# Kernel tuning notes

Hardware: AMD Instinct MI355X
Metric: run time of the kernel (lower is better)

Reference implementation:

```python
import math
import jax, jax.numpy as jnp
import numpy as np

NUM_HEADS = 12
KEEP_RATE = 0.7


def setup_inputs() -> dict:
    key = jax.random.key(0)
    k1, k2, k3 = jax.random.split(key, 3)
    B, N, C = 16, 577, 768
    x = jax.random.normal(k1, (B, N, C), dtype=jnp.float32)
    qkv_w = jax.random.normal(k2, (3 * C, C), dtype=jnp.float32) * 0.02
    proj_w = jax.random.normal(k3, (C, C), dtype=jnp.float32) * 0.02
    proj_b = jnp.zeros((C,), dtype=jnp.float32)
    return {"x": x, "qkv_w": qkv_w, "proj_w": proj_w, "proj_b": proj_b}


def reference(x, qkv_w, proj_w, proj_b):
    B, N, C = x.shape
    H = NUM_HEADS
    hd = C // H
    scale = hd ** -0.5
    # qkv projection (no bias): [B, N, 3C] -> [3, B, H, N, hd]
    qkv = (x @ qkv_w.T).reshape(B, N, 3, H, hd).transpose(2, 0, 3, 1, 4)
    q, k, v = qkv[0], qkv[1], qkv[2]
    attn = jax.nn.softmax(jnp.einsum('bhnd,bhmd->bhnm', q, k) * scale, axis=-1)
    out = jnp.einsum('bhnm,bhmd->bhnd', attn, v)          # [B,H,N,hd]
    out = out.transpose(0, 2, 1, 3).reshape(B, N, C)
    out = out @ proj_w.T + proj_b
    # CLS-token attention pruning (keep_rate < 1.0, return_idx=True path)
    left_tokens = math.ceil(KEEP_RATE * (N - 1))
    cls_attn = attn[:, :, 0, 1:].mean(axis=1)             # [B, N-1], mean over heads
    _, idx = jax.lax.top_k(cls_attn, left_tokens)         # sorted descending
    index = jnp.broadcast_to(idx[:, :, None], (B, left_tokens, C))
    return out, idx, index, cls_attn
```

## Files before the change

kernel.cpp:

```cpp
#include <hip/hip_runtime.h>
#include <math.h>

#define BB 16
#define NN 577
#define CC 768
#define HH 12
#define HD 64
#define MM (BB*NN)
#define MPAD 9344
#define LEFT 404
#define NPAD 608
#define NQT 10

typedef __attribute__((ext_vector_type(8))) short short8v;
typedef __attribute__((ext_vector_type(4))) float f32x4;

__device__ __forceinline__ unsigned short f2bf(float f) {
    union { float f; unsigned int u; } v; v.f = f;
    unsigned int r = v.u + 0x7fffu + ((v.u >> 16) & 1u);
    return (unsigned short)(r >> 16);
}

__global__ __launch_bounds__(256) void k_gemm_fp32(const float* __restrict__ X,
                                                   const float* __restrict__ W,
                                                   float* __restrict__ kb,
                                                   unsigned short* __restrict__ kbh)
{
    __shared__ float Xs[16][128];
    __shared__ float Ws[16][128];
    const int t  = threadIdx.x;
    const int tx = t & 15, ty = t >> 4;
    const int m0 = blockIdx.x * 128;
    const int n0 = 768 + blockIdx.y * 128;
    const int sm = t & 127;
    const int sk = (t >> 7) * 8;

    float acc[8][8];
    #pragma unroll
    for (int i = 0; i < 8; ++i)
        #pragma unroll
        for (int j = 0; j < 8; ++j) acc[i][j] = 0.f;

    const int gm = m0 + sm;
    const float* px = X + (size_t)gm * CC + sk;
    const float* pw = W + (size_t)(n0 + sm) * CC + sk;

    float4 a0 = make_float4(0.f,0.f,0.f,0.f), a1 = a0, b0, b1;
    if (gm < MM) { a0 = *(const float4*)px; a1 = *(const float4*)(px + 4); }
    b0 = *(const float4*)pw; b1 = *(const float4*)(pw + 4);

    for (int kk = 0; kk < CC; kk += 16) {
        Xs[sk+0][sm] = a0.x; Xs[sk+1][sm] = a0.y; Xs[sk+2][sm] = a0.z; Xs[sk+3][sm] = a0.w;
        Xs[sk+4][sm] = a1.x; Xs[sk+5][sm] = a1.y; Xs[sk+6][sm] = a1.z; Xs[sk+7][sm] = a1.w;
        Ws[sk+0][sm] = b0.x; Ws[sk+1][sm] = b0.y; Ws[sk+2][sm] = b0.z; Ws[sk+3][sm] = b0.w;
        Ws[sk+4][sm] = b1.x; Ws[sk+5][sm] = b1.y; Ws[sk+6][sm] = b1.z; Ws[sk+7][sm] = b1.w;
        __syncthreads();
        if (kk + 16 < CC) {
            a0 = make_float4(0.f,0.f,0.f,0.f); a1 = a0;
            if (gm < MM) { a0 = *(const float4*)(px + kk + 16); a1 = *(const float4*)(px + kk + 20); }
            b0 = *(const float4*)(pw + kk + 16); b1 = *(const float4*)(pw + kk + 20);
        }
        #pragma unroll
        for (int k = 0; k < 16; ++k) {
            float a[8], bv[8];
            *(float4*)&a[0]  = *(const float4*)&Xs[k][ty*4];
            *(float4*)&a[4]  = *(const float4*)&Xs[k][64 + ty*4];
            *(float4*)&bv[0] = *(const float4*)&Ws[k][tx*4];
            *(float4*)&bv[4] = *(const float4*)&Ws[k][64 + tx*4];
            #pragma unroll
            for (int i = 0; i < 8; ++i)
                #pragma unroll
                for (int j = 0; j < 8; ++j)
                    acc[i][j] = fmaf(a[i], bv[j], acc[i][j]);
        }
        __syncthreads();
    }
    #pragma unroll
    for (int i = 0; i < 8; ++i) {
        const int mrow = m0 + ((i < 4) ? (ty*4 + i) : (64 + ty*4 + i - 4));
        if (mrow >= MM) continue;
        const int b_ = mrow / NN;
        const int n_ = mrow - b_ * NN;
        #pragma unroll
        for (int j = 0; j < 8; ++j) {
            const int col = (n0 - 768) + ((j < 4) ? (tx*4 + j) : (64 + tx*4 + j - 4));
            const int h = col >> 6, d = col & 63;
            const float a = acc[i][j];
            kb [(((size_t)b_ * HH + h) * NN   + n_) * HD + d] = a;
            kbh[(((size_t)b_ * HH + h) * NPAD + n_) * HD + d] = f2bf(a);
        }
    }
}

__global__ __launch_bounds__(256) void qcls_kernel(const float* __restrict__ X,
                                                   const float* __restrict__ W,
                                                   float* __restrict__ qcls)
{
    const int b = blockIdx.x;
    const int col = blockIdx.y * 256 + threadIdx.x;
    const float* xr = X + (size_t)b * NN * CC;
    const float* wr = W + (size_t)col * CC;
    float acc = 0.f;
    for (int k = 0; k < CC; ++k) acc = fmaf(xr[k], wr[k], acc);
    qcls[(size_t)b * CC + col] = acc;
}

#define N4X 1772544
#define N4W 442368
#define N4P 147456
__global__ __launch_bounds__(256) void convert3(const float* __restrict__ x,
                                                const float* __restrict__ wq,
                                                const float* __restrict__ wp,
                                                unsigned short* __restrict__ xb,
                                                unsigned short* __restrict__ wqb,
                                                unsigned short* __restrict__ wpb)
{
    int g = blockIdx.x * 256 + threadIdx.x;
    const float* src; unsigned short* dst;
    if (g < N4X)            { src = x;  dst = xb;  }
    else if (g < N4X + N4W) { g -= N4X; src = wq; dst = wqb; }
    else                    { g -= (N4X + N4W); src = wp; dst = wpb; }
    const float4 v = ((const float4*)src)[g];
    ushort4 o;
    o.x = f2bf(v.x); o.y = f2bf(v.y); o.z = f2bf(v.z); o.w = f2bf(v.w);
    ((ushort4*)dst)[g] = o;
}

__global__ __launch_bounds__(256) void qv_mfma(const unsigned short* __restrict__ xbh,
                                               const unsigned short* __restrict__ wqkv,
                                               unsigned short* __restrict__ qbh,
                                               unsigned short* __restrict__ Vt)
{
    __shared__ unsigned short As[128*32];
    __shared__ unsigned short Bs[128*32];
    const int t = threadIdx.x;
    const int w = t >> 6, l = t & 63;
    const int l15 = l & 15, lk = l >> 4;
    const int wm = w >> 1, wn = w & 1;
    const int m0 = blockIdx.x * 128;
    const int isV = blockIdx.y >= 6;
    const int nlocal0 = (isV ? (blockIdx.y - 6) : blockIdx.y) * 128;
    const int wrow0 = (isV ? 1536 : 0) + nlocal0;
    const int r0 = t >> 2, segp = t & 3;

    f32x4 acc[4][4];
    #pragma unroll
    for (int i = 0; i < 4; ++i)
        #pragma unroll
        for (int j = 0; j < 4; ++j) acc[i][j] = (f32x4){0.f,0.f,0.f,0.f};

    const unsigned short* ga = xbh  + (size_t)(m0 + r0) * CC + segp * 8;
    const unsigned short* gb = wqkv + (size_t)(wrow0 + r0) * CC + segp * 8;

    for (int kk = 0; kk < CC; kk += 32) {
        const short8v a0 = *(const short8v*)(ga + kk);
        const short8v a1 = *(const short8v*)(ga + kk + (size_t)64 * CC);
        const short8v b0 = *(const short8v*)(gb + kk);
        const short8v b1 = *(const short8v*)(gb + kk + (size_t)64 * CC);
        __syncthreads();
        *(short8v*)&As[(r0)      * 32 + segp*8] = a0;
        *(short8v*)&As[(64 + r0) * 32 + segp*8] = a1;
        *(short8v*)&Bs[(r0)      * 32 + segp*8] = b0;
        *(short8v*)&Bs[(64 + r0) * 32 + segp*8] = b1;
        __syncthreads();
        short8v fa[4], fb[4];
        #pragma unroll
        for (int i = 0; i < 4; ++i) fa[i] = *(const short8v*)&As[(wm*64 + i*16 + l15)*32 + lk*8];
        #pragma unroll
        for (int j = 0; j < 4; ++j) fb[j] = *(const short8v*)&Bs[(wn*64 + j*16 + l15)*32 + lk*8];
        #pragma unroll
        for (int i = 0; i < 4; ++i)
            #pragma unroll
            for (int j = 0; j < 4; ++j)
                acc[i][j] = __builtin_amdgcn_mfma_f32_16x16x32_bf16(fa[i], fb[j], acc[i][j], 0, 0, 0);
    }

    const int nb = nlocal0 + wn*64 + l15;
    #pragma unroll
    for (int i = 0; i < 4; ++i) {
        #pragma unroll
        for (int r = 0; r < 4; ++r) {
            const int m = m0 + wm*64 + i*16 + 4*lk + r;
            if (m >= MM) continue;
            const int b_ = m / NN, tok = m - b_ * NN;
            #pragma unroll
            for (int j = 0; j < 4; ++j) {
                const int nl = nb + j*16;
                const int h = nl >> 6, d = nl & 63;
                const unsigned short v = f2bf(acc[i][j][r]);
                if (isV) Vt [(((size_t)b_*HH + h)*HD + d)*NPAD + tok] = v;
                else     qbh[(((size_t)b_*HH + h)*NPAD + tok)*HD + d] = v;
            }
        }
    }
}

__global__ __launch_bounds__(256) void proj_mfma(const unsigned short* __restrict__ aobh,
                                                 const unsigned short* __restrict__ wpb,
                                                 const float* __restrict__ bias,
                                                 float* __restrict__ outp)
{
    __shared__ unsigned short As[128*32];
    __shared__ unsigned short Bs[128*32];
    const int t = threadIdx.x;
    const int w = t >> 6, l = t & 63;
    const int l15 = l & 15, lk = l >> 4;
    const int wm = w >> 1, wn = w & 1;
    const int m0 = blockIdx.x * 128;
    const int n0 = blockIdx.y * 128;
    const int r0 = t >> 2, segp = t & 3;

    f32x4 acc[4][4];
    #pragma unroll
    for (int i = 0; i < 4; ++i)
        #pragma unroll
        for (int j = 0; j < 4; ++j) acc[i][j] = (f32x4){0.f,0.f,0.f,0.f};

    const unsigned short* ga = aobh + (size_t)(m0 + r0) * CC + segp * 8;
    const unsigned short* gb = wpb  + (size_t)(n0 + r0) * CC + segp * 8;

    for (int kk = 0; kk < CC; kk += 32) {
        const short8v a0 = *(const short8v*)(ga + kk);
        const short8v a1 = *(const short8v*)(ga + kk + (size_t)64 * CC);
        const short8v b0 = *(const short8v*)(gb + kk);
        const short8v b1 = *(const short8v*)(gb + kk + (size_t)64 * CC);
        __syncthreads();
        *(short8v*)&As[(r0)      * 32 + segp*8] = a0;
        *(short8v*)&As[(64 + r0) * 32 + segp*8] = a1;
        *(short8v*)&Bs[(r0)      * 32 + segp*8] = b0;
        *(short8v*)&Bs[(64 + r0) * 32 + segp*8] = b1;
        __syncthreads();
        short8v fa[4], fb[4];
        #pragma unroll
        for (int i = 0; i < 4; ++i) fa[i] = *(const short8v*)&As[(wm*64 + i*16 + l15)*32 + lk*8];
        #pragma unroll
        for (int j = 0; j < 4; ++j) fb[j] = *(const short8v*)&Bs[(wn*64 + j*16 + l15)*32 + lk*8];
        #pragma unroll
        for (int i = 0; i < 4; ++i)
            #pragma unroll
            for (int j = 0; j < 4; ++j)
                acc[i][j] = __builtin_amdgcn_mfma_f32_16x16x32_bf16(fa[i], fb[j], acc[i][j], 0, 0, 0);
    }

    const int nb = n0 + wn*64 + l15;
    #pragma unroll
    for (int i = 0; i < 4; ++i) {
        #pragma unroll
        for (int r = 0; r < 4; ++r) {
            const int m = m0 + wm*64 + i*16 + 4*lk + r;
            if (m >= MM) continue;
            #pragma unroll
            for (int j = 0; j < 4; ++j) {
                const int n = nb + j*16;
                outp[(size_t)m * CC + n] = acc[i][j][r] + bias[n];
            }
        }
    }
}

__global__ __launch_bounds__(256) void attn_mfma(const unsigned short* __restrict__ qbh,
                                                 const unsigned short* __restrict__ kbh,
                                                 const unsigned short* __restrict__ Vt,
                                                 unsigned short* __restrict__ aobh)
{
    __shared__ __align__(16) unsigned short plds[4][16][32];
    const int bid = blockIdx.x;
    const int bh  = bid / NQT;
    const int qt  = bid - bh * NQT;
    const int b   = bh / HH, h = bh - b * HH;
    const int t   = threadIdx.x;
    const int w   = t >> 6, l = t & 63;
    const int l15 = l & 15, lg = l >> 4;

    short8v aq0, aq1;
    {
        int qrow = qt*64 + w*16 + l15; if (qrow > 576) qrow = 576;
        const unsigned short* qp = qbh + ((size_t)bh * NPAD + qrow) * HD + lg*8;
        aq0 = *(const short8v*)(qp);
        aq1 = *(const short8v*)(qp + 32);
    }

    f32x4 O0 = {0.f,0.f,0.f,0.f}, O1 = O0, O2 = O0, O3 = O0;
    float mr[4] = {-1e30f,-1e30f,-1e30f,-1e30f};
    float lr[4] = {0.f,0.f,0.f,0.f};

    const unsigned short* kwb = kbh + (size_t)bh * NPAD * HD + (size_t)l15 * HD + lg*8;
    const unsigned short* vwb = Vt  + (size_t)bh * HD * NPAD + (size_t)l15 * NPAD + lg*8;

    for (int c = 0; c < 19; ++c) {
        const int n0 = c * 32;
        const unsigned short* kp = kwb + (size_t)n0 * HD;
        short8v bk00 = *(const short8v*)(kp);
        short8v bk01 = *(const short8v*)(kp + 32);
        short8v bk10 = *(const short8v*)(kp + 16*HD);
        short8v bk11 = *(const short8v*)(kp + 16*HD + 32);
        f32x4 s0 = {0.f,0.f,0.f,0.f}, s1 = {0.f,0.f,0.f,0.f};
        s0 = __builtin_amdgcn_mfma_f32_16x16x32_bf16(aq0, bk00, s0, 0, 0, 0);
        s0 = __builtin_amdgcn_mfma_f32_16x16x32_bf16(aq1, bk01, s0, 0, 0, 0);
        s1 = __builtin_amdgcn_mfma_f32_16x16x32_bf16(aq0, bk10, s1, 0, 0, 0);
        s1 = __builtin_amdgcn_mfma_f32_16x16x32_bf16(aq1, bk11, s1, 0, 0, 0);

        const int nc0 = n0 + l15;
        float p0[4], p1[4], al[4];
        #pragma unroll
        for (int r = 0; r < 4; ++r) {
            float a0 = (nc0      <= 576) ? s0[r] * 0.125f : -1e30f;
            float a1 = (nc0 + 16 <= 576) ? s1[r] * 0.125f : -1e30f;
            float tm = fmaxf(a0, a1);
            tm = fmaxf(tm, __shfl_xor(tm, 1, 64));
            tm = fmaxf(tm, __shfl_xor(tm, 2, 64));
            tm = fmaxf(tm, __shfl_xor(tm, 4, 64));
            tm = fmaxf(tm, __shfl_xor(tm, 8, 64));
            const float mn = fmaxf(mr[r], tm);
            al[r] = __expf(mr[r] - mn);
            mr[r] = mn;
            p0[r] = __expf(a0 - mn);
            p1[r] = __expf(a1 - mn);
            float ps = p0[r] + p1[r];
            ps += __shfl_xor(ps, 1, 64);
            ps += __shfl_xor(ps, 2, 64);
            ps += __shfl_xor(ps, 4, 64);
            ps += __shfl_xor(ps, 8, 64);
            lr[r] = lr[r] * al[r] + ps;
        }
        #pragma unroll
        for (int r = 0; r < 4; ++r) {
            O0[r] *= al[r]; O1[r] *= al[r]; O2[r] *= al[r]; O3[r] *= al[r];
        }
        #pragma unroll
        for (int r = 0; r < 4; ++r) {
            plds[w][lg*4 + r][l15]      = f2bf(p0[r]);
            plds[w][lg*4 + r][16 + l15] = f2bf(p1[r]);
        }
        asm volatile("s_waitcnt lgkmcnt(0)" ::: "memory");
        short8v pa = *(const short8v*)&plds[w][l15][lg*8];
        const unsigned short* vp = vwb + n0;
        short8v v0 = *(const short8v*)(vp);
        short8v v1 = *(const short8v*)(vp + 16*NPAD);
        short8v v2 = *(const short8v*)(vp + 32*NPAD);
        short8v v3 = *(const short8v*)(vp + 48*NPAD);
        O0 = __builtin_amdgcn_mfma_f32_16x16x32_bf16(pa, v0, O0, 0, 0, 0);
        O1 = __builtin_amdgcn_mfma_f32_16x16x32_bf16(pa, v1, O1, 0, 0, 0);
        O2 = __builtin_amdgcn_mfma_f32_16x16x32_bf16(pa, v2, O2, 0, 0, 0);
        O3 = __builtin_amdgcn_mfma_f32_16x16x32_bf16(pa, v3, O3, 0, 0, 0);
    }

    #pragma unroll
    for (int r = 0; r < 4; ++r) {
        const float inv = 1.f / lr[r];
        const int row = qt*64 + w*16 + lg*4 + r;
        if (row <= 576) {
            unsigned short* op = aobh + ((size_t)b * NN + row) * CC + h*HD + l15;
            op[0]  = f2bf(O0[r] * inv);
            op[16] = f2bf(O1[r] * inv);
            op[32] = f2bf(O2[r] * inv);
            op[48] = f2bf(O3[r] * inv);
        }
    }
}

__global__ __launch_bounds__(256) void cls_logits(const float* __restrict__ qcls,
                                                  const float* __restrict__ kb,
                                                  float* __restrict__ P)
{
    const int bh = blockIdx.x;
    const int t = threadIdx.x;
    __shared__ float q[64];
    if (t < 64) q[t] = qcls[(size_t)bh * 64 + t];
    __syncthreads();
    const int n = blockIdx.y * 193 + t;
    if (t < 193 && n < NN) {
        const float* kr = kb + ((size_t)bh * NN + n) * HD;
        float acc = 0.f;
        #pragma unroll
        for (int d = 0; d < 64; ++d) acc = fmaf(q[d], kr[d], acc);
        P[(size_t)bh * NN + n] = acc * 0.125f;
    }
}

__global__ __launch_bounds__(256) void cls_softmax(float* __restrict__ P)
{
    const int bh = blockIdx.x;
    const int t = threadIdx.x;
    float* L = P + (size_t)bh * NN;
    __shared__ float red[256];
    float lmax = -1e30f;
    for (int n = t; n < NN; n += 256) lmax = fmaxf(lmax, L[n]);
    red[t] = lmax; __syncthreads();
    for (int s = 128; s > 0; s >>= 1) { if (t < s) red[t] = fmaxf(red[t], red[t+s]); __syncthreads(); }
    const float m = red[0]; __syncthreads();
    float z = 0.f;
    for (int n = t; n < NN; n += 256) z += expf(L[n] - m);
    red[t] = z; __syncthreads();
    for (int s = 128; s > 0; s >>= 1) { if (t < s) red[t] += red[t+s]; __syncthreads(); }
    const float Z = red[0];
    for (int n = t; n < NN; n += 256) L[n] = expf(L[n] - m) / Z;
}

__global__ __launch_bounds__(256) void cls_meantopk(const float* __restrict__ P,
                                                    float* __restrict__ out_cls,
                                                    float* __restrict__ out_idx,
                                                    int* __restrict__ idxi)
{
    const int b = blockIdx.x;
    const int t = threadIdx.x;
    __shared__ float sv[576];
    for (int j = t; j < 576; j += 256) {
        float s = 0.f;
        #pragma unroll
        for (int h = 0; h < HH; ++h) s += P[((size_t)(b * HH + h)) * NN + 1 + j];
        const float v = s / 12.0f;
        sv[j] = v;
        out_cls[b * 576 + j] = v;
    }
    __syncthreads();
    for (int i = t; i < 576; i += 256) {
        const float vi = sv[i];
        int rank = 0;
        for (int j = 0; j < 576; ++j) {
            const float vj = sv[j];
            if (vj > vi || (vj == vi && j < i)) ++rank;
        }
        if (rank < LEFT) {
            out_idx[(size_t)b * LEFT + rank] = (float)i;
            idxi[(size_t)b * LEFT + rank] = i;
        }
    }
}

__global__ void write_index(const int* __restrict__ idxi, float* __restrict__ out_index)
{
    const int g4 = blockIdx.x * 256 + threadIdx.x;
    const float v = (float)idxi[g4 / 192];
    float4 o; o.x = v; o.y = v; o.z = v; o.w = v;
    ((float4*)out_index)[g4] = o;
}

extern "C" void kernel_launch(void* const* d_in, const int* in_sizes, int n_in,
                              void* d_out, int out_size, void* d_ws, size_t ws_size,
                              hipStream_t stream)
{
    const float* x      = (const float*)d_in[0];
    const float* qkv_w  = (const float*)d_in[1];
    const float* proj_w = (const float*)d_in[2];
    const float* proj_b = (const float*)d_in[3];
    float* out = (float*)d_out;

    char* base = (char*)d_ws;
    float*          kb    = (float*)(base + 0);
    unsigned short* xbh   = (unsigned short*)(base +  28360704);
    unsigned short* qbh   = (unsigned short*)(base +  42713088);
    unsigned short* kbh   = (unsigned short*)(base +  57655296);
    unsigned short* Vt    = (unsigned short*)(base +  72597504);
    unsigned short* aobh  = (unsigned short*)(base +  87539712);
    unsigned short* wqkv  = (unsigned short*)(base + 101892096);
    unsigned short* wpb   = (unsigned short*)(base + 105431040);
    float*          qcls  = (float*)(base + 106610688);
    float*          P     = (float*)(base + 106659840);
    int*            idxi  = (int*)  (base + 107139840);

    float* out_main  = out;
    float* out_idx   = out + 7090176;
    float* out_index = out + 7096640;
    float* out_cls   = out + 12060992;

    convert3<<<9228, 256, 0, stream>>>(x, qkv_w, proj_w, xbh, wqkv, wpb);
    qcls_kernel<<<dim3(16, 3), 256, 0, stream>>>(x, qkv_w, qcls);
    k_gemm_fp32<<<dim3(73, 6), 256, 0, stream>>>(x, qkv_w, kb, kbh);
    qv_mfma<<<dim3(73, 12), 256, 0, stream>>>(xbh, wqkv, qbh, Vt);
    attn_mfma<<<BB * HH * NQT, 256, 0, stream>>>(qbh, kbh, Vt, aobh);
    proj_mfma<<<dim3(73, 6), 256, 0, stream>>>(aobh, wpb, proj_b, out_main);

    cls_logits<<<dim3(BB * HH, 3), 256, 0, stream>>>(qcls, kb, P);
    cls_softmax<<<BB * HH, 256, 0, stream>>>(P);
    cls_meantopk<<<BB, 256, 0, stream>>>(P, out_cls, out_idx, idxi);
    write_index<<<4848, 256, 0, stream>>>(idxi, out_index);
}
```

Measured before the change: 437.5 us.

## Double-buffer QKV and projection GEMM tiles with direct global-to-LDS loads

The bf16 MFMA GEMMs for the Q/V projection and the output projection now use two LDS buffers per operand. Tiles are filled with global_load_lds, which writes straight from global memory into shared memory without staging through registers. The next K-slice is issued before the current slice is computed, and one barrier per iteration replaces the previous two. The aim is to hide global load latency behind MFMA work and to cut register pressure and barrier count, at the cost of doubling the LDS footprint per block.

```diff
diff --git a/kernel.cpp b/kernel.cpp
--- a/kernel.cpp
+++ b/kernel.cpp
@@ -20,6 +20,11 @@
     unsigned int r = v.u + 0x7fffu + ((v.u >> 16) & 1u);
     return (unsigned short)(r >> 16);
 }
+
+#define GLDS16(gp, lp)                                                        \
+    __builtin_amdgcn_global_load_lds(                                         \
+        (const __attribute__((address_space(1))) void*)(gp),                  \
+        (__attribute__((address_space(3))) void*)(lp), 16, 0, 0)
 
 __global__ __launch_bounds__(256) void k_gemm_fp32(const float* __restrict__ X,
                                                    const float* __restrict__ W,
@@ -131,8 +136,8 @@
                                                unsigned short* __restrict__ qbh,
                                                unsigned short* __restrict__ Vt)
 {
-    __shared__ unsigned short As[128*32];
-    __shared__ unsigned short Bs[128*32];
+    __shared__ unsigned short As[2][4096];
+    __shared__ unsigned short Bs[2][4096];
     const int t = threadIdx.x;
     const int w = t >> 6, l = t & 63;
     const int l15 = l & 15, lk = l >> 4;
@@ -151,29 +156,35 @@
 
     const unsigned short* ga = xbh  + (size_t)(m0 + r0) * CC + segp * 8;
     const unsigned short* gb = wqkv + (size_t)(wrow0 + r0) * CC + segp * 8;
-
+    const int wbase = w * 512;
+
+    #define QV_STAGE(bb, kk)                                                  \
+        do {                                                                  \
+            GLDS16(ga + (kk),                   &As[bb][wbase]);              \
+            GLDS16(ga + (kk) + (size_t)64 * CC, &As[bb][2048 + wbase]);       \
+            GLDS16(gb + (kk),                   &Bs[bb][wbase]);              \
+            GLDS16(gb + (kk) + (size_t)64 * CC, &Bs[bb][2048 + wbase]);       \
+        } while (0)
+
+    QV_STAGE(0, 0);
+    __syncthreads();
+    int cur = 0;
     for (int kk = 0; kk < CC; kk += 32) {
-        const short8v a0 = *(const short8v*)(ga + kk);
-        const short8v a1 = *(const short8v*)(ga + kk + (size_t)64 * CC);
-        const short8v b0 = *(const short8v*)(gb + kk);
-        const short8v b1 = *(const short8v*)(gb + kk + (size_t)64 * CC);
-        __syncthreads();
-        *(short8v*)&As[(r0)      * 32 + segp*8] = a0;
-        *(short8v*)&As[(64 + r0) * 32 + segp*8] = a1;
-        *(short8v*)&Bs[(r0)      * 32 + segp*8] = b0;
-        *(short8v*)&Bs[(64 + r0) * 32 + segp*8] = b1;
-        __syncthreads();
+        if (kk + 32 < CC) QV_STAGE(cur ^ 1, kk + 32);
         short8v fa[4], fb[4];
         #pragma unroll
-        for (int i = 0; i < 4; ++i) fa[i] = *(const short8v*)&As[(wm*64 + i*16 + l15)*32 + lk*8];
-        #pragma unroll
-        for (int j = 0; j < 4; ++j) fb[j] = *(const short8v*)&Bs[(wn*64 + j*16 + l15)*32 + lk*8];
+        for (int i = 0; i < 4; ++i) fa[i] = *(const short8v*)&As[cur][(wm*64 + i*16 + l15)*32 + lk*8];
+        #pragma unroll
+        for (int j = 0; j < 4; ++j) fb[j] = *(const short8v*)&Bs[cur][(wn*64 + j*16 + l15)*32 + lk*8];
         #pragma unroll
         for (int i = 0; i < 4; ++i)
             #pragma unroll
             for (int j = 0; j < 4; ++j)
                 acc[i][j] = __builtin_amdgcn_mfma_f32_16x16x32_bf16(fa[i], fb[j], acc[i][j], 0, 0, 0);
-    }
+        __syncthreads();
+        cur ^= 1;
+    }
+    #undef QV_STAGE
 
     const int nb = nlocal0 + wn*64 + l15;
     #pragma unroll
@@ -200,8 +211,8 @@
                                                  const float* __restrict__ bias,
                                                  float* __restrict__ outp)
 {
-    __shared__ unsigned short As[128*32];
-    __shared__ unsigned short Bs[128*32];
+    __shared__ unsigned short As[2][4096];
+    __shared__ unsigned short Bs[2][4096];
     const int t = threadIdx.x;
     const int w = t >> 6, l = t & 63;
     const int l15 = l & 15, lk = l >> 4;
@@ -218,29 +229,35 @@
 
     const unsigned short* ga = aobh + (size_t)(m0 + r0) * CC + segp * 8;
     const unsigned short* gb = wpb  + (size_t)(n0 + r0) * CC + segp * 8;
-
+    const int wbase = w * 512;
+
+    #define PJ_STAGE(bb, kk)                                                  \
+        do {                                                                  \
+            GLDS16(ga + (kk),                   &As[bb][wbase]);              \
+            GLDS16(ga + (kk) + (size_t)64 * CC, &As[bb][2048 + wbase]);       \
+            GLDS16(gb + (kk),                   &Bs[bb][wbase]);              \
+            GLDS16(gb + (kk) + (size_t)64 * CC, &Bs[bb][2048 + wbase]);       \
+        } while (0)
+
+    PJ_STAGE(0, 0);
+    __syncthreads();
+    int cur = 0;
     for (int kk = 0; kk < CC; kk += 32) {
-        const short8v a0 = *(const short8v*)(ga + kk);
-        const short8v a1 = *(const short8v*)(ga + kk + (size_t)64 * CC);
-        const short8v b0 = *(const short8v*)(gb + kk);
-        const short8v b1 = *(const short8v*)(gb + kk + (size_t)64 * CC);
-        __syncthreads();
-        *(short8v*)&As[(r0)      * 32 + segp*8] = a0;
-        *(short8v*)&As[(64 + r0) * 32 + segp*8] = a1;
-        *(short8v*)&Bs[(r0)      * 32 + segp*8] = b0;
-        *(short8v*)&Bs[(64 + r0) * 32 + segp*8] = b1;
-        __syncthreads();
+        if (kk + 32 < CC) PJ_STAGE(cur ^ 1, kk + 32);
         short8v fa[4], fb[4];
         #pragma unroll
-        for (int i = 0; i < 4; ++i) fa[i] = *(const short8v*)&As[(wm*64 + i*16 + l15)*32 + lk*8];
-        #pragma unroll
-        for (int j = 0; j < 4; ++j) fb[j] = *(const short8v*)&Bs[(wn*64 + j*16 + l15)*32 + lk*8];
+        for (int i = 0; i < 4; ++i) fa[i] = *(const short8v*)&As[cur][(wm*64 + i*16 + l15)*32 + lk*8];
+        #pragma unroll
+        for (int j = 0; j < 4; ++j) fb[j] = *(const short8v*)&Bs[cur][(wn*64 + j*16 + l15)*32 + lk*8];
         #pragma unroll
         for (int i = 0; i < 4; ++i)
             #pragma unroll
             for (int j = 0; j < 4; ++j)
                 acc[i][j] = __builtin_amdgcn_mfma_f32_16x16x32_bf16(fa[i], fb[j], acc[i][j], 0, 0, 0);
-    }
+        __syncthreads();
+        cur ^= 1;
+    }
+    #undef PJ_STAGE
 
     const int nb = n0 + wn*64 + l15;
     #pragma unroll
```

New measurement: 441.5 us. About the same (+0.9%).
